# Performance work log

Measured on AMD Instinct MI355X. Metric: run time of the kernel, lower is better.

Reference implementation:

```python
import jax, jax.numpy as jnp
import numpy as np

DIM = 192
D_STATE = 16
D_CONV = 4
EXPAND = 2
D_INNER = DIM * EXPAND          # 384
DT_RANK = (DIM + 15) // 16      # 12
B_SZ, H_SP, W_SP = 4, 64, 64


def setup_inputs() -> dict:
    key = jax.random.key(0)
    ks = jax.random.split(key, 8)
    f = jax.random.normal
    return {
        "x": f(ks[0], (B_SZ, DIM, H_SP, W_SP), jnp.float32),
        "ln_w": jnp.ones((DIM,), jnp.float32),
        "ln_b": jnp.zeros((DIM,), jnp.float32),
        "in_proj_w": f(ks[1], (2 * D_INNER, DIM), jnp.float32) * 0.02,
        "conv_w": f(ks[2], (D_INNER, D_CONV), jnp.float32) * 0.2,
        "conv_b": jnp.zeros((D_INNER,), jnp.float32),
        "x_proj_w": f(ks[3], (DT_RANK + 2 * D_STATE, D_INNER), jnp.float32) * 0.02,
        "dt_proj_w": f(ks[4], (D_INNER, DT_RANK), jnp.float32) * 0.1,
        "dt_proj_b": f(ks[5], (D_INNER,), jnp.float32) * 0.1,
        "A_log": jnp.log(jnp.broadcast_to(
            jnp.arange(1, D_STATE + 1, dtype=jnp.float32), (D_INNER, D_STATE))),
        "D": jnp.ones((D_INNER,), jnp.float32),
        "out_proj_w": f(ks[6], (DIM, D_INNER), jnp.float32) * 0.02,
    }


def _mamba_block(x, ln_w, ln_b, in_proj_w, conv_w, conv_b, x_proj_w,
                 dt_proj_w, dt_proj_b, A_log, D, out_proj_w):
    B, C, H, W = x.shape
    L = H * W
    # [B,C,H,W] -> [B,L,C]
    xf = x.transpose(0, 2, 3, 1).reshape(B, L, C)

    # LayerNorm
    mu = xf.mean(-1, keepdims=True)
    var = ((xf - mu) ** 2).mean(-1, keepdims=True)
    xn = (xf - mu) * jax.lax.rsqrt(var + 1e-5) * ln_w + ln_b

    # in_proj -> xm (ssm branch), z (gate branch)
    xz = xn @ in_proj_w.T                      # [B,L,2*Di]
    xm, z = jnp.split(xz, 2, axis=-1)

    # causal depthwise conv1d over sequence (pad left d_conv-1)
    xc = xm.transpose(0, 2, 1)                 # [B,Di,L]
    xc = jax.lax.conv_general_dilated(
        xc, conv_w[:, None, :], (1,), [(D_CONV - 1, 0)],
        dimension_numbers=("NCH", "OIH", "NCH"),
        feature_group_count=D_INNER)
    xc = xc + conv_b[None, :, None]
    xm = jax.nn.silu(xc.transpose(0, 2, 1))    # [B,L,Di]

    # x_proj -> dt, B, C (input-dependent SSM params)
    dbc = xm @ x_proj_w.T                      # [B,L,dt_rank+2N]
    dt, Bm, Cm = jnp.split(dbc, [DT_RANK, DT_RANK + D_STATE], axis=-1)
    dt = jax.nn.softplus(dt @ dt_proj_w.T + dt_proj_b)  # [B,L,Di]

    A = -jnp.exp(A_log)                        # [Di,N]

    def step(h, inp):
        xt, dtt, Bt, Ct = inp                  # [B,Di],[B,Di],[B,N],[B,N]
        dA = jnp.exp(dtt[..., None] * A)       # [B,Di,N]
        h = h * dA + (dtt * xt)[..., None] * Bt[:, None, :]
        y = jnp.einsum('bdn,bn->bd', h, Ct)
        return h, y

    h0 = jnp.zeros((B, D_INNER, D_STATE), xm.dtype)
    scan_in = (xm.transpose(1, 0, 2), dt.transpose(1, 0, 2),
               Bm.transpose(1, 0, 2), Cm.transpose(1, 0, 2))
    _, ys = jax.lax.scan(step, h0, scan_in)    # [L,B,Di]

    y = ys.transpose(1, 0, 2) + xm * D         # skip term D*x
    y = y * jax.nn.silu(z)                     # gate
    out = y @ out_proj_w.T                     # [B,L,C]

    out = xf + out                             # residual
    return out.reshape(B, H, W, C).transpose(0, 3, 1, 2)


def reference(x, ln_w, ln_b, in_proj_w, conv_w, conv_b, x_proj_w,
              dt_proj_w, dt_proj_b, A_log, D, out_proj_w):
    return _mamba_block(x, ln_w, ln_b, in_proj_w, conv_w, conv_b, x_proj_w,
                        dt_proj_w, dt_proj_b, A_log, D, out_proj_w)
```

## Files before the change

### kernel.cpp

```cpp
#include <hip/hip_runtime.h>
#include <hip/hip_bf16.h>
#include <cstdint>
#include <cmath>

#define DIMC   192
#define DSTATE 16
#define DCONV  4
#define DINNER 384
#define DTRANK 12
#define BSZ    4
#define HSP    64
#define WSP    64
#define LSEQ   4096
#define NTOK   (BSZ*LSEQ)
#define XZW    (2*DINNER)
#define LC4    16
#define NCH4   (LSEQ/LC4)
#define NXP    448

typedef unsigned short ushortT;
using short8 = __attribute__((ext_vector_type(8))) short;
using f32x4  = __attribute__((ext_vector_type(4))) float;

typedef unsigned int u32_as1 __attribute__((address_space(1)));
typedef unsigned int u32_as3 __attribute__((address_space(3)));

__device__ __forceinline__ void gl_lds16(const ushortT* g, ushortT* l) {
  __builtin_amdgcn_global_load_lds((const u32_as1*)g, (u32_as3*)l, 16, 0, 0);
}

__device__ __forceinline__ float bflo(unsigned u) { return __uint_as_float(u << 16); }
__device__ __forceinline__ float bfhi(unsigned u) { return __uint_as_float(u & 0xffff0000u); }
__device__ __forceinline__ float bf2f(ushortT u) { return __uint_as_float(((unsigned)u) << 16); }
__device__ __forceinline__ unsigned pkbf(float lo, float hi) {
  __hip_bfloat16 l = __float2bfloat16(lo), h = __float2bfloat16(hi);
  return (unsigned)*(ushortT*)&l | ((unsigned)*(ushortT*)&h << 16);
}
#define UNPK8(arr, base, v4)                                        \
  arr[base + 0] = bflo(v4.x); arr[base + 1] = bfhi(v4.x);           \
  arr[base + 2] = bflo(v4.y); arr[base + 3] = bfhi(v4.y);           \
  arr[base + 4] = bflo(v4.z); arr[base + 5] = bfhi(v4.z);           \
  arr[base + 6] = bflo(v4.w); arr[base + 7] = bfhi(v4.w);

__global__ __launch_bounds__(256) void prep_kernel(
    const float* __restrict__ w_in, const float* __restrict__ w_out,
    const float* __restrict__ xpw, const float* __restrict__ dtw,
    __hip_bfloat16* __restrict__ wbf, __hip_bfloat16* __restrict__ wcb) {
  int gid = blockIdx.x * 256 + threadIdx.x;
  if (gid < 221184) {
    float v = gid < 147456 ? w_in[gid] : w_out[gid - 147456];
    wbf[gid] = __float2bfloat16(v);
  } else {
    int e = gid - 221184;
    int dd = e / 384, k = e % 384;
    float v = 0.f;
    if (dd < 384) {
#pragma unroll
      for (int j = 0; j < 12; ++j) v = fmaf(dtw[dd * 12 + j], xpw[j * 384 + k], v);
    } else if (dd < 416) {
      v = xpw[(dd - 372) * 384 + k];
    }
    wcb[e] = __float2bfloat16(v);
  }
}

__global__ __launch_bounds__(512) void ln_kernel(
    const float* __restrict__ x, const float* __restrict__ ln_w,
    const float* __restrict__ ln_b, __hip_bfloat16* __restrict__ xn) {
  __shared__ float xs[DIMC][WSP + 1];
  __shared__ float mu_s[WSP], rs_s[WSP];
  int bh = blockIdx.x;
  int b = bh >> 6, h = bh & 63;
  int tid = threadIdx.x;
  const float* xb = x + (size_t)b * DIMC * LSEQ + (size_t)h * WSP;
  for (int e = tid; e < DIMC * WSP; e += 512) {
    int c = e >> 6, w = e & 63;
    xs[c][w] = xb[(size_t)c * LSEQ + w];
  }
  __syncthreads();
  {
    int w = tid >> 3, p = tid & 7;
    float s = 0.f, s2 = 0.f;
#pragma unroll
    for (int i = 0; i < 24; ++i) {
      float v = xs[p * 24 + i][w];
      s += v; s2 = fmaf(v, v, s2);
    }
    s  += __shfl_xor(s, 1);  s2 += __shfl_xor(s2, 1);
    s  += __shfl_xor(s, 2);  s2 += __shfl_xor(s2, 2);
    s  += __shfl_xor(s, 4);  s2 += __shfl_xor(s2, 4);
    if (p == 0) {
      float mu = s * (1.f / DIMC);
      float var = s2 * (1.f / DIMC) - mu * mu;
      mu_s[w] = mu;
      rs_s[w] = rsqrtf(var + 1e-5f);
    }
  }
  __syncthreads();
  __hip_bfloat16* xo = xn + (size_t)(b * LSEQ + h * WSP) * DIMC;
  for (int e = tid; e < DIMC * WSP; e += 512) {
    int w = e / DIMC, c = e % DIMC;
    xo[(size_t)w * DIMC + c] =
        __float2bfloat16((xs[c][w] - mu_s[w]) * rs_s[w] * ln_w[c] + ln_b[c]);
  }
}

template<int WM, int WN, int FM, int FN, int EPI>
__global__ __launch_bounds__(256) void gemm_bf16(
    const ushortT* __restrict__ A, const ushortT* __restrict__ B,
    void* __restrict__ Cv, void* __restrict__ Cv2,
    const ushortT* __restrict__ xm_aux, const float* __restrict__ bias384,
    const float* __restrict__ xres, int K, int Nreal, int ldc) {
  constexpr int BM = WM * FM * 16, BN = WN * FN * 16;
  __shared__ ushortT As[BM][64];
  __shared__ ushortT Bs[BN][64];
  __shared__ float Ct[(EPI == 1) ? (BM * (BN + 4)) : 1];
  int bm = blockIdx.x * BM, bn = blockIdx.y * BN;
  int tid = threadIdx.x, lane = tid & 63, w = tid >> 6;
  int wm = w / WN, wn = w % WN;
  int lm = lane & 15, lk = lane >> 4;
  int sub = lane >> 3, slot = lane & 7;
  const ushortT* Bb = B;
  size_t zoff = 0;
  if constexpr (EPI == 1) {
    size_t zb = blockIdx.z;
    Bb = B + zb * (size_t)LSEQ * K;
    zoff = zb * (size_t)DIMC * LSEQ;
  }
  f32x4 acc[FM][FN];
#pragma unroll
  for (int mi = 0; mi < FM; ++mi)
#pragma unroll
    for (int ni = 0; ni < FN; ++ni) acc[mi][ni] = (f32x4){0.f, 0.f, 0.f, 0.f};

  for (int k0 = 0; k0 < K; k0 += 64) {
    __syncthreads();
#pragma unroll
    for (int j = 0; j < BM / 32; ++j) {
      int row = w * (BM / 4) + j * 8;
      gl_lds16(A + (size_t)(bm + row + sub) * K + k0 + ((slot ^ sub) << 3),
               &As[row][0]);
    }
#pragma unroll
    for (int j = 0; j < BN / 32; ++j) {
      int row = w * (BN / 4) + j * 8;
      gl_lds16(Bb + (size_t)(bn + row + sub) * K + k0 + ((slot ^ sub) << 3),
               &Bs[row][0]);
    }
    __syncthreads();
#pragma unroll
    for (int ks = 0; ks < 2; ++ks) {
      short8 af[FM], bfr[FN];
#pragma unroll
      for (int mi = 0; mi < FM; ++mi) {
        int row = wm * FM * 16 + mi * 16 + lm;
        int col = (ks * 64 + lk * 16) ^ ((lm & 7) << 4);
        af[mi] = *(const short8*)((const char*)As + row * 128 + col);
      }
#pragma unroll
      for (int ni = 0; ni < FN; ++ni) {
        int row = wn * FN * 16 + ni * 16 + lm;
        int col = (ks * 64 + lk * 16) ^ ((lm & 7) << 4);
        bfr[ni] = *(const short8*)((const char*)Bs + row * 128 + col);
      }
#pragma unroll
      for (int mi = 0; mi < FM; ++mi)
#pragma unroll
        for (int ni = 0; ni < FN; ++ni)
          acc[mi][ni] = __builtin_amdgcn_mfma_f32_16x16x32_bf16(
              af[mi], bfr[ni], acc[mi][ni], 0, 0, 0);
    }
  }

  if constexpr (EPI == 1) {
    __syncthreads();
    float (*CtA)[BN + 4] = (float(*)[BN + 4])Ct;
#pragma unroll
    for (int mi = 0; mi < FM; ++mi)
#pragma unroll
      for (int ni = 0; ni < FN; ++ni)
#pragma unroll
        for (int r = 0; r < 4; ++r)
          CtA[wm * FM * 16 + mi * 16 + lk * 4 + r][wn * FN * 16 + ni * 16 + lm] =
              acc[mi][ni][r];
    __syncthreads();
    float* Cout = (float*)Cv;
    for (int e = tid; e < BM * (BN / 4); e += 256) {
      int row = e / (BN / 4), q = e % (BN / 4);
      size_t gidx = zoff + (size_t)(bm + row) * LSEQ + bn + q * 4;
      float4 rv = *(const float4*)(xres + gidx);
      float4 o;
      o.x = CtA[row][q * 4 + 0] + rv.x;
      o.y = CtA[row][q * 4 + 1] + rv.y;
      o.z = CtA[row][q * 4 + 2] + rv.z;
      o.w = CtA[row][q * 4 + 3] + rv.w;
      *(float4*)(Cout + gidx) = o;
    }
  } else {
#pragma unroll
    for (int mi = 0; mi < FM; ++mi) {
#pragma unroll
      for (int ni = 0; ni < FN; ++ni) {
        int ncol = bn + wn * FN * 16 + ni * 16 + lm;
#pragma unroll
        for (int r = 0; r < 4; ++r) {
          int m = bm + wm * FM * 16 + mi * 16 + lk * 4 + r;
          if constexpr (EPI == 2) {
            if (ncol < Nreal)
              ((__hip_bfloat16*)Cv)[(size_t)m * ldc + ncol] =
                  __float2bfloat16(acc[mi][ni][r]);
          } else {
            if (ncol < 384) {
              float dtr = acc[mi][ni][r] + bias384[ncol];
              float dt = dtr > 15.f ? dtr : __logf(1.f + __expf(dtr));
              float xmv = bf2f(xm_aux[(size_t)m * DINNER + ncol]);
              ((unsigned*)Cv)[(size_t)m * DINNER + ncol] = pkbf(dt, xmv);
            } else if (ncol < 416) {
              __hip_bfloat16 bv = __float2bfloat16(acc[mi][ni][r]);
              ((ushortT*)Cv2)[(size_t)m * 48 + 16 + (ncol - 384)] = *(ushortT*)&bv;
            }
          }
        }
      }
    }
  }
}

__global__ __launch_bounds__(256) void conv_silu_kernel(
    const __hip_bfloat16* __restrict__ xz, const float* __restrict__ conv_w,
    const float* __restrict__ conv_b, __hip_bfloat16* __restrict__ xmh) {
  int g8 = blockIdx.x * 256 + threadIdx.x;
  int d8 = g8 % 48;
  int tok = g8 / 48;
  int l = tok & (LSEQ - 1);
  int d0 = d8 * 8;
  const ushortT* base = (const ushortT*)xz + (size_t)tok * XZW + d0;
  uint4 r0, r1, r2, r3;
  r3 = *(const uint4*)(base);
  r2 = l >= 1 ? *(const uint4*)(base - XZW)     : (uint4){0, 0, 0, 0};
  r1 = l >= 2 ? *(const uint4*)(base - 2 * XZW) : (uint4){0, 0, 0, 0};
  r0 = l >= 3 ? *(const uint4*)(base - 3 * XZW) : (uint4){0, 0, 0, 0};
  float x0[8], x1[8], x2[8], x3[8];
  UNPK8(x0, 0, r0) UNPK8(x1, 0, r1) UNPK8(x2, 0, r2) UNPK8(x3, 0, r3)
  ushortT outv[8];
#pragma unroll
  for (int j = 0; j < 8; ++j) {
    const float4 w = *(const float4*)(conv_w + (d0 + j) * 4);
    float acc = conv_b[d0 + j];
    acc = fmaf(w.x, x0[j], acc);
    acc = fmaf(w.y, x1[j], acc);
    acc = fmaf(w.z, x2[j], acc);
    acc = fmaf(w.w, x3[j], acc);
    float s = acc / (1.f + __expf(-acc));
    __hip_bfloat16 sb = __float2bfloat16(s);
    outv[j] = *(ushortT*)&sb;
  }
  *(uint4*)((ushortT*)xmh + (size_t)tok * DINNER + d0) = *(uint4*)outv;
}

__global__ __launch_bounds__(384) void scan_part1(
    const unsigned* __restrict__ dxpk, const ushortT* __restrict__ dbc,
    const float* __restrict__ A_log, unsigned* __restrict__ hpk) {
  __shared__ ushortT dbc_s[16 * 48];
  int d = threadIdx.x, c = blockIdx.x, b = blockIdx.y;
  size_t rowbase = (size_t)b * LSEQ + (size_t)c * LC4;
  if (d < 96) {
    int row = d / 6, q = d % 6;
    ((uint4*)dbc_s)[d] = ((const uint4*)(dbc + (rowbase + row) * 48))[q];
  }
  float Ac2[16];
#pragma unroll
  for (int q = 0; q < 4; ++q) {
    float4 t4 = *(const float4*)(A_log + d * 16 + q * 4);
    Ac2[q * 4 + 0] = -__expf(t4.x) * 1.44269504f;
    Ac2[q * 4 + 1] = -__expf(t4.y) * 1.44269504f;
    Ac2[q * 4 + 2] = -__expf(t4.z) * 1.44269504f;
    Ac2[q * 4 + 3] = -__expf(t4.w) * 1.44269504f;
  }
  float h[16];
#pragma unroll
  for (int n = 0; n < 16; ++n) h[n] = 0.f;
  float sdt = 0.f;
  const unsigned* pkp = dxpk + rowbase * DINNER + d;
  __syncthreads();
#pragma unroll
  for (int t0 = 0; t0 < 16; t0 += 4) {
    unsigned pk[4];
#pragma unroll
    for (int j = 0; j < 4; ++j) pk[j] = pkp[(t0 + j) * DINNER];
#pragma unroll
    for (int j = 0; j < 4; ++j) {
      int t = t0 + j;
      float dtt = bflo(pk[j]), xmv = bfhi(pk[j]);
      sdt += dtt;
      float dx = dtt * xmv;
      const char* bb = (const char*)dbc_s + t * 96;
      uint4 B0 = *(const uint4*)(bb + 32);
      uint4 B1 = *(const uint4*)(bb + 48);
      float Bv[16];
      UNPK8(Bv, 0, B0)
      UNPK8(Bv, 8, B1)
#pragma unroll
      for (int n = 0; n < 16; ++n) {
        float a = __builtin_amdgcn_exp2f(dtt * Ac2[n]);
        h[n] = fmaf(h[n], a, dx * Bv[n]);
      }
    }
  }
  unsigned up[16];
#pragma unroll
  for (int n = 0; n < 16; ++n)
    up[n] = pkbf(h[n], __builtin_amdgcn_exp2f(Ac2[n] * sdt));
  uint4* hp4 = (uint4*)(hpk + (((size_t)b * NCH4 + c) * DINNER + d) * 16);
#pragma unroll
  for (int q = 0; q < 4; ++q) hp4[q] = *(uint4*)&up[q * 4];
}

__global__ __launch_bounds__(256) void scan_part2(
    const unsigned* __restrict__ hpk, ushortT* __restrict__ hinb) {
  int e = blockIdx.x * 256 + threadIdx.x;
  int b = blockIdx.y;
  float H = 0.f;
  size_t base = (size_t)b * NCH4 * (DINNER * DSTATE) + e;
#pragma unroll 16
  for (int c = 0; c < NCH4; ++c) {
    size_t idx = base + (size_t)c * (DINNER * DSTATE);
    unsigned w = hpk[idx];
    __hip_bfloat16 hb = __float2bfloat16(H);
    hinb[idx] = *(ushortT*)&hb;
    H = fmaf(bfhi(w), H, bflo(w));
  }
}

__global__ __launch_bounds__(384) void scan_part3(
    const unsigned* __restrict__ dxpk, const ushortT* __restrict__ dbc,
    const __hip_bfloat16* __restrict__ xz, const float* __restrict__ A_log,
    const float* __restrict__ Dvec, const ushortT* __restrict__ hinb,
    __hip_bfloat16* __restrict__ ybuf) {
  __shared__ ushortT dbc_s[16 * 48];
  int d = threadIdx.x, c = blockIdx.x, b = blockIdx.y;
  size_t rowbase = (size_t)b * LSEQ + (size_t)c * LC4;
  if (d < 96) {
    int row = d / 6, q = d % 6;
    ((uint4*)dbc_s)[d] = ((const uint4*)(dbc + (rowbase + row) * 48))[q];
  }
  float Ac2[16];
#pragma unroll
  for (int q = 0; q < 4; ++q) {
    float4 t4 = *(const float4*)(A_log + d * 16 + q * 4);
    Ac2[q * 4 + 0] = -__expf(t4.x) * 1.44269504f;
    Ac2[q * 4 + 1] = -__expf(t4.y) * 1.44269504f;
    Ac2[q * 4 + 2] = -__expf(t4.z) * 1.44269504f;
    Ac2[q * 4 + 3] = -__expf(t4.w) * 1.44269504f;
  }
  float h[16];
  {
    const uint4* hp = (const uint4*)(hinb + (((size_t)b * NCH4 + c) * DINNER + d) * 16);
    uint4 h0 = hp[0], h1 = hp[1];
    UNPK8(h, 0, h0)
    UNPK8(h, 8, h1)
  }
  float Dd = Dvec[d];
  const unsigned* pkp = dxpk + rowbase * DINNER + d;
  const ushortT* zp = (const ushortT*)xz + rowbase * XZW + DINNER + d;
  __hip_bfloat16* yp = ybuf + rowbase * DINNER + d;
  __syncthreads();
#pragma unroll
  for (int t0 = 0; t0 < 16; t0 += 4) {
    unsigned pk[4];
    ushortT zv4[4];
#pragma unroll
    for (int j = 0; j < 4; ++j) {
      pk[j] = pkp[(t0 + j) * DINNER];
      zv4[j] = zp[(t0 + j) * XZW];
    }
#pragma unroll
    for (int j = 0; j < 4; ++j) {
      int t = t0 + j;
      float dtt = bflo(pk[j]), xmv = bfhi(pk[j]);
      float dx = dtt * xmv;
      const char* bb = (const char*)dbc_s + t * 96;
      uint4 B0 = *(const uint4*)(bb + 32);
      uint4 B1 = *(const uint4*)(bb + 48);
      uint4 C0 = *(const uint4*)(bb + 64);
      uint4 C1 = *(const uint4*)(bb + 80);
      float Bv[16], Cw[16];
      UNPK8(Bv, 0, B0)
      UNPK8(Bv, 8, B1)
      UNPK8(Cw, 0, C0)
      UNPK8(Cw, 8, C1)
      float y0 = 0.f, y1 = 0.f, y2 = 0.f, y3 = 0.f;
#pragma unroll
      for (int n = 0; n < 16; n += 4) {
        float a0 = __builtin_amdgcn_exp2f(dtt * Ac2[n + 0]);
        float a1 = __builtin_amdgcn_exp2f(dtt * Ac2[n + 1]);
        float a2 = __builtin_amdgcn_exp2f(dtt * Ac2[n + 2]);
        float a3 = __builtin_amdgcn_exp2f(dtt * Ac2[n + 3]);
        h[n + 0] = fmaf(h[n + 0], a0, dx * Bv[n + 0]);
        h[n + 1] = fmaf(h[n + 1], a1, dx * Bv[n + 1]);
        h[n + 2] = fmaf(h[n + 2], a2, dx * Bv[n + 2]);
        h[n + 3] = fmaf(h[n + 3], a3, dx * Bv[n + 3]);
        y0 = fmaf(h[n + 0], Cw[n + 0], y0);
        y1 = fmaf(h[n + 1], Cw[n + 1], y1);
        y2 = fmaf(h[n + 2], Cw[n + 2], y2);
        y3 = fmaf(h[n + 3], Cw[n + 3], y3);
      }
      float yv = fmaf(xmv, Dd, (y0 + y1) + (y2 + y3));
      float zv = bf2f(zv4[j]);
      float gt = zv * __builtin_amdgcn_rcpf(
          1.f + __builtin_amdgcn_exp2f(zv * -1.44269504f));
      yp[(size_t)t * DINNER] = __float2bfloat16(yv * gt);
    }
  }
}

extern "C" void kernel_launch(void* const* d_in, const int* in_sizes, int n_in,
                              void* d_out, int out_size, void* d_ws, size_t ws_size,
                              hipStream_t stream) {
  const float* x        = (const float*)d_in[0];
  const float* ln_w     = (const float*)d_in[1];
  const float* ln_b     = (const float*)d_in[2];
  const float* in_proj  = (const float*)d_in[3];
  const float* conv_w   = (const float*)d_in[4];
  const float* conv_b   = (const float*)d_in[5];
  const float* x_proj   = (const float*)d_in[6];
  const float* dt_w     = (const float*)d_in[7];
  const float* dt_b     = (const float*)d_in[8];
  const float* A_log    = (const float*)d_in[9];
  const float* Dvec     = (const float*)d_in[10];
  const float* out_proj = (const float*)d_in[11];
  float* out = (float*)d_out;

  float* ws = (float*)d_ws;
  __hip_bfloat16* xzb  = (__hip_bfloat16*)ws;
  __hip_bfloat16* xmh  = (__hip_bfloat16*)(ws + 6291456);
  ushortT*        dbcb = (ushortT*)(ws + 9437184);
  unsigned*       dxpk = (unsigned*)(ws + 9830400);
  unsigned*       hpk  = (unsigned*)(ws + 16121856);
  ushortT*        hinb = (ushortT*)(ws + 22413312);
  __hip_bfloat16* ybuf = (__hip_bfloat16*)(ws + 25559040);
  __hip_bfloat16* xnbf = (__hip_bfloat16*)(ws + 28704768);
  __hip_bfloat16* wbf  = (__hip_bfloat16*)(ws + 30277632);
  __hip_bfloat16* wcb  = (__hip_bfloat16*)(ws + 30388224);

  const ushortT* win  = (const ushortT*)wbf;
  const ushortT* wout = (const ushortT*)(wbf + 147456);

  prep_kernel<<<1536, 256, 0, stream>>>(in_proj, out_proj, x_proj, dt_w, wbf, wcb);

  ln_kernel<<<BSZ * HSP, 512, 0, stream>>>(x, ln_w, ln_b, xnbf);

  gemm_bf16<2, 2, 4, 4, 2><<<dim3(NTOK / 128, XZW / 128), 256, 0, stream>>>(
      (const ushortT*)xnbf, win, xzb, nullptr, nullptr, nullptr, nullptr,
      DIMC, XZW, XZW);

  conv_silu_kernel<<<(NTOK * DINNER / 8) / 256, 256, 0, stream>>>(
      xzb, conv_w, conv_b, xmh);

  gemm_bf16<2, 2, 4, 2, 4><<<dim3(NTOK / 128, NXP / 64), 256, 0, stream>>>(
      (const ushortT*)xmh, (const ushortT*)wcb, dxpk, dbcb,
      (const ushortT*)xmh, dt_b, nullptr, DINNER, NXP, 0);

  scan_part1<<<dim3(NCH4, BSZ), 384, 0, stream>>>(dxpk, dbcb, A_log, hpk);
  scan_part2<<<dim3(DINNER * DSTATE / 256, BSZ), 256, 0, stream>>>(hpk, hinb);
  scan_part3<<<dim3(NCH4, BSZ), 384, 0, stream>>>(
      dxpk, dbcb, xzb, A_log, Dvec, hinb, ybuf);

  gemm_bf16<2, 2, 2, 4, 1><<<dim3(DIMC / 64, LSEQ / 128, BSZ), 256, 0, stream>>>(
      wout, (const ushortT*)ybuf, out, nullptr, nullptr, nullptr, x,
      DINNER, LSEQ, LSEQ);
}
```

Before: 154.8 us.

## Merge weight prep into LayerNorm kernel and double scan chunk length

Folds the weight conversion/prep kernel into the LayerNorm kernel as extra blocks, removing one launch. The chunked scan now uses 32-token chunks instead of 16, halving the number of chunk states written and read by the sequential cross-chunk pass and shrinking workspace. The cost is fewer blocks for scan parts 1 and 3 (512 instead of 1024), so there is less parallelism and each thread runs a longer serial loop.

```diff
diff --git a/kernel.cpp b/kernel.cpp
--- a/kernel.cpp
+++ b/kernel.cpp
@@ -14,8 +14,8 @@
 #define LSEQ   4096
 #define NTOK   (BSZ*LSEQ)
 #define XZW    (2*DINNER)
-#define LC4    16
-#define NCH4   (LSEQ/LC4)
+#define LC5    32
+#define NCH5   (LSEQ/LC5)
 #define NXP    448
 
 typedef unsigned short ushortT;
@@ -42,31 +42,31 @@
   arr[base + 4] = bflo(v4.z); arr[base + 5] = bfhi(v4.z);           \
   arr[base + 6] = bflo(v4.w); arr[base + 7] = bfhi(v4.w);
 
-__global__ __launch_bounds__(256) void prep_kernel(
-    const float* __restrict__ w_in, const float* __restrict__ w_out,
-    const float* __restrict__ xpw, const float* __restrict__ dtw,
+__global__ __launch_bounds__(512) void ln_prep_kernel(
+    const float* __restrict__ x, const float* __restrict__ ln_w,
+    const float* __restrict__ ln_b, const float* __restrict__ w_in,
+    const float* __restrict__ w_out, const float* __restrict__ xpw,
+    const float* __restrict__ dtw, __hip_bfloat16* __restrict__ xn,
     __hip_bfloat16* __restrict__ wbf, __hip_bfloat16* __restrict__ wcb) {
-  int gid = blockIdx.x * 256 + threadIdx.x;
-  if (gid < 221184) {
-    float v = gid < 147456 ? w_in[gid] : w_out[gid - 147456];
-    wbf[gid] = __float2bfloat16(v);
-  } else {
-    int e = gid - 221184;
-    int dd = e / 384, k = e % 384;
-    float v = 0.f;
-    if (dd < 384) {
-#pragma unroll
-      for (int j = 0; j < 12; ++j) v = fmaf(dtw[dd * 12 + j], xpw[j * 384 + k], v);
-    } else if (dd < 416) {
-      v = xpw[(dd - 372) * 384 + k];
-    }
-    wcb[e] = __float2bfloat16(v);
-  }
-}
-
-__global__ __launch_bounds__(512) void ln_kernel(
-    const float* __restrict__ x, const float* __restrict__ ln_w,
-    const float* __restrict__ ln_b, __hip_bfloat16* __restrict__ xn) {
+  if (blockIdx.x >= 256) {
+    int gid = (blockIdx.x - 256) * 512 + threadIdx.x;
+    if (gid < 221184) {
+      float v = gid < 147456 ? w_in[gid] : w_out[gid - 147456];
+      wbf[gid] = __float2bfloat16(v);
+    } else {
+      int e = gid - 221184;
+      int dd = e / 384, k = e % 384;
+      float v = 0.f;
+      if (dd < 384) {
+#pragma unroll
+        for (int j = 0; j < 12; ++j) v = fmaf(dtw[dd * 12 + j], xpw[j * 384 + k], v);
+      } else if (dd < 416) {
+        v = xpw[(dd - 372) * 384 + k];
+      }
+      wcb[e] = __float2bfloat16(v);
+    }
+    return;
+  }
   __shared__ float xs[DIMC][WSP + 1];
   __shared__ float mu_s[WSP], rs_s[WSP];
   int bh = blockIdx.x;
@@ -261,10 +261,10 @@
 __global__ __launch_bounds__(384) void scan_part1(
     const unsigned* __restrict__ dxpk, const ushortT* __restrict__ dbc,
     const float* __restrict__ A_log, unsigned* __restrict__ hpk) {
-  __shared__ ushortT dbc_s[16 * 48];
+  __shared__ ushortT dbc_s[32 * 48];
   int d = threadIdx.x, c = blockIdx.x, b = blockIdx.y;
-  size_t rowbase = (size_t)b * LSEQ + (size_t)c * LC4;
-  if (d < 96) {
+  size_t rowbase = (size_t)b * LSEQ + (size_t)c * LC5;
+  if (d < 192) {
     int row = d / 6, q = d % 6;
     ((uint4*)dbc_s)[d] = ((const uint4*)(dbc + (rowbase + row) * 48))[q];
   }
@@ -284,7 +284,7 @@
   const unsigned* pkp = dxpk + rowbase * DINNER + d;
   __syncthreads();
 #pragma unroll
-  for (int t0 = 0; t0 < 16; t0 += 4) {
+  for (int t0 = 0; t0 < LC5; t0 += 4) {
     unsigned pk[4];
 #pragma unroll
     for (int j = 0; j < 4; ++j) pk[j] = pkp[(t0 + j) * DINNER];
@@ -311,7 +311,7 @@
 #pragma unroll
   for (int n = 0; n < 16; ++n)
     up[n] = pkbf(h[n], __builtin_amdgcn_exp2f(Ac2[n] * sdt));
-  uint4* hp4 = (uint4*)(hpk + (((size_t)b * NCH4 + c) * DINNER + d) * 16);
+  uint4* hp4 = (uint4*)(hpk + (((size_t)b * NCH5 + c) * DINNER + d) * 16);
 #pragma unroll
   for (int q = 0; q < 4; ++q) hp4[q] = *(uint4*)&up[q * 4];
 }
@@ -321,9 +321,9 @@
   int e = blockIdx.x * 256 + threadIdx.x;
   int b = blockIdx.y;
   float H = 0.f;
-  size_t base = (size_t)b * NCH4 * (DINNER * DSTATE) + e;
+  size_t base = (size_t)b * NCH5 * (DINNER * DSTATE) + e;
 #pragma unroll 16
-  for (int c = 0; c < NCH4; ++c) {
+  for (int c = 0; c < NCH5; ++c) {
     size_t idx = base + (size_t)c * (DINNER * DSTATE);
     unsigned w = hpk[idx];
     __hip_bfloat16 hb = __float2bfloat16(H);
@@ -337,10 +337,10 @@
     const __hip_bfloat16* __restrict__ xz, const float* __restrict__ A_log,
     const float* __restrict__ Dvec, const ushortT* __restrict__ hinb,
     __hip_bfloat16* __restrict__ ybuf) {
-  __shared__ ushortT dbc_s[16 * 48];
+  __shared__ ushortT dbc_s[32 * 48];
   int d = threadIdx.x, c = blockIdx.x, b = blockIdx.y;
-  size_t rowbase = (size_t)b * LSEQ + (size_t)c * LC4;
-  if (d < 96) {
+  size_t rowbase = (size_t)b * LSEQ + (size_t)c * LC5;
+  if (d < 192) {
     int row = d / 6, q = d % 6;
     ((uint4*)dbc_s)[d] = ((const uint4*)(dbc + (rowbase + row) * 48))[q];
   }
@@ -355,7 +355,7 @@
   }
   float h[16];
   {
-    const uint4* hp = (const uint4*)(hinb + (((size_t)b * NCH4 + c) * DINNER + d) * 16);
+    const uint4* hp = (const uint4*)(hinb + (((size_t)b * NCH5 + c) * DINNER + d) * 16);
     uint4 h0 = hp[0], h1 = hp[1];
     UNPK8(h, 0, h0)
     UNPK8(h, 8, h1)
@@ -366,7 +366,7 @@
   __hip_bfloat16* yp = ybuf + rowbase * DINNER + d;
   __syncthreads();
 #pragma unroll
-  for (int t0 = 0; t0 < 16; t0 += 4) {
+  for (int t0 = 0; t0 < LC5; t0 += 4) {
     unsigned pk[4];
     ushortT zv4[4];
 #pragma unroll
@@ -437,18 +437,17 @@
   ushortT*        dbcb = (ushortT*)(ws + 9437184);
   unsigned*       dxpk = (unsigned*)(ws + 9830400);
   unsigned*       hpk  = (unsigned*)(ws + 16121856);
-  ushortT*        hinb = (ushortT*)(ws + 22413312);
-  __hip_bfloat16* ybuf = (__hip_bfloat16*)(ws + 25559040);
-  __hip_bfloat16* xnbf = (__hip_bfloat16*)(ws + 28704768);
-  __hip_bfloat16* wbf  = (__hip_bfloat16*)(ws + 30277632);
-  __hip_bfloat16* wcb  = (__hip_bfloat16*)(ws + 30388224);
+  ushortT*        hinb = (ushortT*)(ws + 19267584);
+  __hip_bfloat16* ybuf = (__hip_bfloat16*)(ws + 20840448);
+  __hip_bfloat16* xnbf = (__hip_bfloat16*)(ws + 23986176);
+  __hip_bfloat16* wbf  = (__hip_bfloat16*)(ws + 25559040);
+  __hip_bfloat16* wcb  = (__hip_bfloat16*)(ws + 25669632);
 
   const ushortT* win  = (const ushortT*)wbf;
   const ushortT* wout = (const ushortT*)(wbf + 147456);
 
-  prep_kernel<<<1536, 256, 0, stream>>>(in_proj, out_proj, x_proj, dt_w, wbf, wcb);
-
-  ln_kernel<<<BSZ * HSP, 512, 0, stream>>>(x, ln_w, ln_b, xnbf);
+  ln_prep_kernel<<<1024, 512, 0, stream>>>(
+      x, ln_w, ln_b, in_proj, out_proj, x_proj, dt_w, xnbf, wbf, wcb);
 
   gemm_bf16<2, 2, 4, 4, 2><<<dim3(NTOK / 128, XZW / 128), 256, 0, stream>>>(
       (const ushortT*)xnbf, win, xzb, nullptr, nullptr, nullptr, nullptr,
@@ -461,9 +460,9 @@
       (const ushortT*)xmh, (const ushortT*)wcb, dxpk, dbcb,
       (const ushortT*)xmh, dt_b, nullptr, DINNER, NXP, 0);
 
-  scan_part1<<<dim3(NCH4, BSZ), 384, 0, stream>>>(dxpk, dbcb, A_log, hpk);
+  scan_part1<<<dim3(NCH5, BSZ), 384, 0, stream>>>(dxpk, dbcb, A_log, hpk);
   scan_part2<<<dim3(DINNER * DSTATE / 256, BSZ), 256, 0, stream>>>(hpk, hinb);
-  scan_part3<<<dim3(NCH4, BSZ), 384, 0, stream>>>(
+  scan_part3<<<dim3(NCH5, BSZ), 384, 0, stream>>>(
       dxpk, dbcb, xzb, A_log, Dvec, hinb, ybuf);
 
   gemm_bf16<2, 2, 2, 4, 1><<<dim3(DIMC / 64, LSEQ / 128, BSZ), 256, 0, stream>>>(
```

After: 141.9 us. -8.3%, faster.
